# Optimization experiments

Hardware: AMD Instinct MI355X
Metric: run time of the kernel (lower is better)

The kernel has to match this reference:

```python
import jax, jax.numpy as jnp
import numpy as np

B, T, D = 2, 4096, 512
H = 8  # heads; head_dim = D // H = 64


def setup_inputs() -> dict:
    key = jax.random.key(0)
    ks = jax.random.split(key, 8)
    s = 0.02
    return {
        "queries": jax.random.normal(ks[0], (B, T, D), jnp.float32),
        "keys": jax.random.normal(ks[1], (B, T, D), jnp.float32),
        "values": jax.random.normal(ks[2], (B, T, D), jnp.float32),
        "Wq": jax.random.normal(ks[3], (D, D), jnp.float32) * s,
        "Wk": jax.random.normal(ks[4], (D, D), jnp.float32) * s,
        "Wv": jax.random.normal(ks[5], (D, D), jnp.float32) * s,
        "Wo": jax.random.normal(ks[6], (D, D), jnp.float32) * s,
        "bo": jnp.zeros((D,), jnp.float32),
    }


def reference(queries, keys, values, Wq, Wk, Wv, Wo, bo):
    # pad_dim = 0 for in_dim=512, n_heads=8, so no padding needed.
    Bq, Tq, _ = queries.shape
    Ts = keys.shape[1]
    hd = D // H
    # torch Linear: x @ W.T
    q = (queries @ Wq.T).reshape(Bq, Tq, H, hd).transpose(0, 2, 1, 3)  # [B,H,T,hd]
    k = (keys @ Wk.T).reshape(Bq, Ts, H, hd).transpose(0, 2, 1, 3)
    v = (values @ Wv.T).reshape(Bq, Ts, H, hd).transpose(0, 2, 1, 3)
    attn = jnp.einsum("bhtd,bhsd->bhts", q, k) / np.sqrt(hd).astype(np.float32)
    attn = jax.nn.softmax(attn, axis=-1)  # [B,H,T,Ts]
    z = jnp.einsum("bhts,bhsd->bhtd", attn, v)
    z = z.transpose(0, 2, 1, 3).reshape(Bq, Tq, D)
    out = z @ Wo.T + bo
    return (out, attn)
```

## Files before the change

### kernel.cpp

```cpp
#include <hip/hip_runtime.h>

typedef __attribute__((ext_vector_type(8))) short bf16x8;
typedef __attribute__((ext_vector_type(8))) unsigned short u16x8;
typedef __attribute__((ext_vector_type(4))) float f32x4;
typedef __attribute__((ext_vector_type(2))) unsigned uint2v;
typedef __attribute__((ext_vector_type(4))) unsigned uint4v;

#define DEVINL __device__ __forceinline__

constexpr int TB = 2;
constexpr int TT = 4096;
constexpr int TD = 512;
constexpr int TH = 8;
constexpr int THD = 64;
constexpr int TM = TB * TT;

DEVINL unsigned short f2b(float f) {
  unsigned u = __builtin_bit_cast(unsigned, f);
  u += 0x7FFFu + ((u >> 16) & 1u);
  return (unsigned short)(u >> 16);
}

DEVINL unsigned cvtpk(float lo, float hi) {
  unsigned r;
  asm("v_cvt_pk_bf16_f32 %0, %1, %2" : "=v"(r) : "v"(lo), "v"(hi));
  return r;
}

DEVINL void lgkm_barrier() {
  asm volatile("s_waitcnt lgkmcnt(0)" ::: "memory");
  __builtin_amdgcn_s_barrier();
  __builtin_amdgcn_sched_barrier(0);
}

template<int MODE>
__global__ __launch_bounds__(256, 2)
void gemm_xwt(const float* __restrict__ X, const float* __restrict__ W,
              unsigned short* __restrict__ Yb, float* __restrict__ Yf,
              const float* __restrict__ bias)
{
  constexpr int K = TD, N = TD;
  __shared__ unsigned short As[128][72];
  __shared__ unsigned short Bs[128][72];

  const int t    = threadIdx.x;
  const int lane = t & 63, w = t >> 6;
  const int fr = lane & 15, fq = lane >> 4;
  const int wr = (w >> 1) * 64, wc = (w & 1) * 64;
  const int bm = blockIdx.x * 128, bn = blockIdx.y * 128;
  const int srow = t >> 1;
  const int skh  = (t & 1) * 32;

  f32x4 acc[4][4];
  #pragma unroll
  for (int i = 0; i < 4; ++i)
    #pragma unroll
    for (int j = 0; j < 4; ++j)
      acc[i][j] = f32x4{0.f, 0.f, 0.f, 0.f};

  for (int k0 = 0; k0 < K; k0 += 64) {
    const float* srcA = X + (size_t)(bm + srow) * K + k0 + skh;
    const float* srcB = W + (size_t)(bn + srow) * K + k0 + skh;
    #pragma unroll
    for (int i = 0; i < 4; ++i) {
      float4 a0 = ((const float4*)srcA)[2 * i];
      float4 a1 = ((const float4*)srcA)[2 * i + 1];
      u16x8 oa = {f2b(a0.x), f2b(a0.y), f2b(a0.z), f2b(a0.w),
                  f2b(a1.x), f2b(a1.y), f2b(a1.z), f2b(a1.w)};
      *(u16x8*)&As[srow][skh + i * 8] = oa;
      float4 b0 = ((const float4*)srcB)[2 * i];
      float4 b1 = ((const float4*)srcB)[2 * i + 1];
      u16x8 ob = {f2b(b0.x), f2b(b0.y), f2b(b0.z), f2b(b0.w),
                  f2b(b1.x), f2b(b1.y), f2b(b1.z), f2b(b1.w)};
      *(u16x8*)&Bs[srow][skh + i * 8] = ob;
    }
    __syncthreads();
    #pragma unroll
    for (int kk = 0; kk < 2; ++kk) {
      bf16x8 af[4], bfv[4];
      #pragma unroll
      for (int i = 0; i < 4; ++i)
        af[i] = *(const bf16x8*)&As[wr + i * 16 + fr][kk * 32 + fq * 8];
      #pragma unroll
      for (int j = 0; j < 4; ++j)
        bfv[j] = *(const bf16x8*)&Bs[wc + j * 16 + fr][kk * 32 + fq * 8];
      #pragma unroll
      for (int i = 0; i < 4; ++i)
        #pragma unroll
        for (int j = 0; j < 4; ++j) {
          if (MODE == 2)
            acc[i][j] = __builtin_amdgcn_mfma_f32_16x16x32_bf16(bfv[i], af[j], acc[i][j], 0, 0, 0);
          else
            acc[i][j] = __builtin_amdgcn_mfma_f32_16x16x32_bf16(af[i], bfv[j], acc[i][j], 0, 0, 0);
        }
    }
    __syncthreads();
  }

  #pragma unroll
  for (int i = 0; i < 4; ++i) {
    #pragma unroll
    for (int j = 0; j < 4; ++j) {
      #pragma unroll
      for (int ii = 0; ii < 4; ++ii) {
        float v = acc[i][j][ii];
        if (MODE == 2) {
          const int Nidx = bn + wc + i * 16 + fq * 4 + ii;
          const int Midx = bm + wr + j * 16 + fr;
          const int h = Nidx >> 6, d = Nidx & (THD - 1);
          const int b = Midx >> 12, tt = Midx & (TT - 1);
          Yb[((size_t)(b * TH + h) * THD + d) * TT + tt] = f2b(v);
        } else {
          const int gm = bm + wr + i * 16 + fq * 4 + ii;
          const int gn = bn + wc + j * 16 + fr;
          if (MODE == 1) Yf[(size_t)gm * N + gn] = v + bias[gn];
          else           Yb[(size_t)gm * N + gn] = f2b(v);
        }
      }
    }
  }
}

__global__ __launch_bounds__(256, 2)
void attn_fused(const unsigned short* __restrict__ Qb,
                const unsigned short* __restrict__ Kb,
                const unsigned short* __restrict__ VTg,
                float* __restrict__ attnO, float* __restrict__ Z)
{
  __shared__ __align__(16) char smem_[55552];
  auto Ks   = (unsigned short (*)[64][72])smem_;
  auto VTs  = (unsigned short (*)[64][72])(smem_ + 18432);
  float* Lred = (float*)(smem_ + 55296);
  auto Zs   = (float (*)[68])smem_;

  const int t    = threadIdx.x;
  const int lane = t & 63, w = t >> 6;
  const int fr = lane & 15, fq = lane >> 4;
  const int bh = blockIdx.y;
  const int b  = bh >> 3, h = bh & 7;
  const int q0 = blockIdx.x * 64;

  const size_t rowKV  = ((size_t)(b * TT)) * TD + h * THD;
  const size_t vtBase = (size_t)bh * THD * TT;

  const int tr = t >> 2;
  const int tc = (t & 3) * 16;

  auto loadK = [&](int kvt, u16x8& r0, u16x8& r1) {
    const unsigned short* src = Kb + rowKV + (size_t)(kvt * 64 + tr) * TD + tc;
    r0 = *(const u16x8*)src;
    r1 = *(const u16x8*)(src + 8);
  };
  auto loadVT = [&](int kvt, u16x8& r0, u16x8& r1) {
    const unsigned short* src = VTg + vtBase + (size_t)tr * TT + kvt * 64 + tc;
    r0 = *(const u16x8*)src;
    r1 = *(const u16x8*)(src + 8);
  };
  auto writeK = [&](int buf, const u16x8& r0, const u16x8& r1) {
    *(u16x8*)&Ks[buf][tr][tc]     = r0;
    *(u16x8*)&Ks[buf][tr][tc + 8] = r1;
  };
  auto writeVT = [&](int buf, const u16x8& r0, const u16x8& r1) {
    *(u16x8*)&VTs[buf][tr][tc]     = r0;
    *(u16x8*)&VTs[buf][tr][tc + 8] = r1;
  };

  bf16x8 aq[4][2];
  #pragma unroll
  for (int qf = 0; qf < 4; ++qf) {
    const unsigned short* qsrc =
        Qb + ((size_t)(b * TT + q0 + qf * 16 + fr)) * TD + h * THD;
    aq[qf][0] = *(const bf16x8*)(qsrc + fq * 8);
    aq[qf][1] = *(const bf16x8*)(qsrc + 32 + fq * 8);
  }

  constexpr int NT = TT / 64;
  constexpr float K2 = 0.18033688011112042f;

  u16x8 kr0, kr1, vr0, vr1;
  loadK(0, kr0, kr1);
  writeK(0, kr0, kr1);
  lgkm_barrier();

  float lsum[4] = {0.f, 0.f, 0.f, 0.f};
  for (int j = 0; j < NT; ++j) {
    const int cur = j & 1;
    if (j + 1 < NT) loadK(j + 1, kr0, kr1);
    bf16x8 ak0 = *(const bf16x8*)&Ks[cur][w * 16 + fr][fq * 8];
    bf16x8 ak1 = *(const bf16x8*)&Ks[cur][w * 16 + fr][32 + fq * 8];
    __builtin_amdgcn_s_setprio(1);
    #pragma unroll
    for (int qf = 0; qf < 4; ++qf) {
      f32x4 s = f32x4{0.f, 0.f, 0.f, 0.f};
      s = __builtin_amdgcn_mfma_f32_16x16x32_bf16(ak0, aq[qf][0], s, 0, 0, 0);
      s = __builtin_amdgcn_mfma_f32_16x16x32_bf16(ak1, aq[qf][1], s, 0, 0, 0);
      #pragma unroll
      for (int i = 0; i < 4; ++i)
        lsum[qf] += __builtin_amdgcn_exp2f(s[i] * K2);
    }
    __builtin_amdgcn_s_setprio(0);
    if (j + 1 < NT) writeK(cur ^ 1, kr0, kr1);
    lgkm_barrier();
  }
  #pragma unroll
  for (int qf = 0; qf < 4; ++qf) {
    lsum[qf] += __shfl_xor(lsum[qf], 16, 64);
    lsum[qf] += __shfl_xor(lsum[qf], 32, 64);
  }
  if (fq == 0) {
    #pragma unroll
    for (int qf = 0; qf < 4; ++qf)
      Lred[(w * 4 + qf) * 16 + fr] = lsum[qf];
  }
  __syncthreads();
  float l2i[4];
  #pragma unroll
  for (int qf = 0; qf < 4; ++qf) {
    float s = Lred[(0 * 4 + qf) * 16 + fr] + Lred[(1 * 4 + qf) * 16 + fr] +
              Lred[(2 * 4 + qf) * 16 + fr] + Lred[(3 * 4 + qf) * 16 + fr];
    l2i[qf] = -__log2f(s);
  }

  loadK(0, kr0, kr1);
  loadVT(0, vr0, vr1);
  writeK(0, kr0, kr1);
  writeVT(0, vr0, vr1);
  lgkm_barrier();

  f32x4 accz[4][4];
  #pragma unroll
  for (int i = 0; i < 4; ++i)
    #pragma unroll
    for (int j = 0; j < 4; ++j)
      accz[i][j] = f32x4{0.f, 0.f, 0.f, 0.f};

  unsigned pa[4][4];

#define QK_TILE(J, HALF)                                                       \
  {                                                                            \
    if ((J) + 1 < NT) { loadK((J) + 1, kr0, kr1); loadVT((J) + 1, vr0, vr1); } \
    bf16x8 ak0 = *(const bf16x8*)&Ks[(J) & 1][w * 16 + fr][fq * 8];            \
    bf16x8 ak1 = *(const bf16x8*)&Ks[(J) & 1][w * 16 + fr][32 + fq * 8];       \
    __builtin_amdgcn_s_setprio(1);                                             \
    _Pragma("unroll")                                                          \
    for (int qf = 0; qf < 4; ++qf) {                                           \
      f32x4 s = f32x4{0.f, 0.f, 0.f, 0.f};                                     \
      s = __builtin_amdgcn_mfma_f32_16x16x32_bf16(ak0, aq[qf][0], s, 0, 0, 0); \
      s = __builtin_amdgcn_mfma_f32_16x16x32_bf16(ak1, aq[qf][1], s, 0, 0, 0); \
      float p0 = __builtin_amdgcn_exp2f(fmaf(s[0], K2, l2i[qf]));              \
      float p1 = __builtin_amdgcn_exp2f(fmaf(s[1], K2, l2i[qf]));              \
      float p2 = __builtin_amdgcn_exp2f(fmaf(s[2], K2, l2i[qf]));              \
      float p3 = __builtin_amdgcn_exp2f(fmaf(s[3], K2, l2i[qf]));              \
      f32x4 pv4 = {p0, p1, p2, p3};                                            \
      __builtin_nontemporal_store(pv4,                                         \
        (f32x4*)(attnO + ((size_t)bh * TT + q0 + qf * 16 + fr) * TT            \
                 + (J) * 64 + w * 16 + fq * 4));                               \
      pa[qf][(HALF) * 2 + 0] = cvtpk(p0, p1);                                  \
      pa[qf][(HALF) * 2 + 1] = cvtpk(p2, p3);                                  \
    }                                                                          \
    __builtin_amdgcn_s_setprio(0);                                             \
  }
#define STAGE_TAIL(J)                                                          \
  {                                                                            \
    if ((J) + 1 < NT) {                                                        \
      writeK(((J) + 1) & 1, kr0, kr1);                                         \
      writeVT(((J) + 1) & 3, vr0, vr1);                                        \
    }                                                                          \
    lgkm_barrier();                                                            \
  }

  for (int jp = 0; jp < NT / 2; ++jp) {
    const int j0 = jp * 2;
    const int vb = (jp & 1) * 2;
    QK_TILE(j0, 0)
    STAGE_TAIL(j0)
    QK_TILE(j0 + 1, 1)
    __builtin_amdgcn_s_setprio(1);
    #pragma unroll
    for (int df = 0; df < 4; ++df) {
      uint2v lo = *(const uint2v*)&VTs[vb][df * 16 + fr][w * 16 + fq * 4];
      uint2v hi = *(const uint2v*)&VTs[vb + 1][df * 16 + fr][w * 16 + fq * 4];
      uint4v bvv = {lo[0], lo[1], hi[0], hi[1]};
      bf16x8 bv = __builtin_bit_cast(bf16x8, bvv);
      #pragma unroll
      for (int qf = 0; qf < 4; ++qf) {
        uint4v pav = {pa[qf][0], pa[qf][1], pa[qf][2], pa[qf][3]};
        accz[qf][df] = __builtin_amdgcn_mfma_f32_16x16x32_bf16(
            __builtin_bit_cast(bf16x8, pav), bv, accz[qf][df], 0, 0, 0);
      }
    }
    __builtin_amdgcn_s_setprio(0);
    STAGE_TAIL(j0 + 1)
  }
#undef QK_TILE
#undef STAGE_TAIL

  for (int ww = 0; ww < 4; ++ww) {
    if (w == ww) {
      #pragma unroll
      for (int qf = 0; qf < 4; ++qf)
        #pragma unroll
        for (int df = 0; df < 4; ++df)
          #pragma unroll
          for (int i = 0; i < 4; ++i) {
            float* zp = &Zs[qf * 16 + fq * 4 + i][df * 16 + fr];
            float v = accz[qf][df][i];
            if (ww != 0) v += *zp;
            *zp = v;
          }
    }
    __syncthreads();
  }
  {
    const int r = t >> 2, c4 = (t & 3) * 16;
    float* zdst = Z + (size_t)(b * TT + q0 + r) * TD + h * THD + c4;
    #pragma unroll
    for (int i = 0; i < 4; ++i)
      *(f32x4*)(zdst + i * 4) = *(const f32x4*)&Zs[r][c4 + i * 4];
  }
}

extern "C" void kernel_launch(void* const* d_in, const int* in_sizes, int n_in,
                              void* d_out, int out_size, void* d_ws, size_t ws_size,
                              hipStream_t stream) {
  const float* queries = (const float*)d_in[0];
  const float* keys    = (const float*)d_in[1];
  const float* values  = (const float*)d_in[2];
  const float* Wq = (const float*)d_in[3];
  const float* Wk = (const float*)d_in[4];
  const float* Wv = (const float*)d_in[5];
  const float* Wo = (const float*)d_in[6];
  const float* bo = (const float*)d_in[7];

  float* out  = (float*)d_out;
  float* attn = out + (size_t)TM * TD;

  unsigned short* qb = (unsigned short*)d_ws;
  unsigned short* kb = qb + (size_t)TM * TD;
  unsigned short* vt = kb + (size_t)TM * TD;
  float*          zf = (float*)(vt + (size_t)TM * TD);

  dim3 gg(TM / 128, TD / 128), bb(256);
  gemm_xwt<0><<<gg, bb, 0, stream>>>(queries, Wq, qb, nullptr, nullptr);
  gemm_xwt<0><<<gg, bb, 0, stream>>>(keys,    Wk, kb, nullptr, nullptr);
  gemm_xwt<2><<<gg, bb, 0, stream>>>(values,  Wv, vt, nullptr, nullptr);

  attn_fused<<<dim3(TT / 64, TB * TH), bb, 0, stream>>>(qb, kb, vt, attn, zf);

  gemm_xwt<1><<<gg, bb, 0, stream>>>(zf, Wo, nullptr, out, bo);
}
```

Measured before the change: 542.9 us.

## Split KV range across waves and load K/V directly from global memory

```diff
diff --git a/kernel.cpp b/kernel.cpp
--- a/kernel.cpp
+++ b/kernel.cpp
@@ -25,12 +25,6 @@
   unsigned r;
   asm("v_cvt_pk_bf16_f32 %0, %1, %2" : "=v"(r) : "v"(lo), "v"(hi));
   return r;
-}
-
-DEVINL void lgkm_barrier() {
-  asm volatile("s_waitcnt lgkmcnt(0)" ::: "memory");
-  __builtin_amdgcn_s_barrier();
-  __builtin_amdgcn_sched_barrier(0);
 }
 
 template<int MODE>
@@ -127,11 +121,8 @@
                 const unsigned short* __restrict__ VTg,
                 float* __restrict__ attnO, float* __restrict__ Z)
 {
-  __shared__ __align__(16) char smem_[55552];
-  auto Ks   = (unsigned short (*)[64][72])smem_;
-  auto VTs  = (unsigned short (*)[64][72])(smem_ + 18432);
-  float* Lred = (float*)(smem_ + 55296);
-  auto Zs   = (float (*)[68])smem_;
+  __shared__ float Lred[4][4][16];
+  __shared__ float Zs[64][68];
 
   const int t    = threadIdx.x;
   const int lane = t & 63, w = t >> 6;
@@ -143,28 +134,6 @@
   const size_t rowKV  = ((size_t)(b * TT)) * TD + h * THD;
   const size_t vtBase = (size_t)bh * THD * TT;
 
-  const int tr = t >> 2;
-  const int tc = (t & 3) * 16;
-
-  auto loadK = [&](int kvt, u16x8& r0, u16x8& r1) {
-    const unsigned short* src = Kb + rowKV + (size_t)(kvt * 64 + tr) * TD + tc;
-    r0 = *(const u16x8*)src;
-    r1 = *(const u16x8*)(src + 8);
-  };
-  auto loadVT = [&](int kvt, u16x8& r0, u16x8& r1) {
-    const unsigned short* src = VTg + vtBase + (size_t)tr * TT + kvt * 64 + tc;
-    r0 = *(const u16x8*)src;
-    r1 = *(const u16x8*)(src + 8);
-  };
-  auto writeK = [&](int buf, const u16x8& r0, const u16x8& r1) {
-    *(u16x8*)&Ks[buf][tr][tc]     = r0;
-    *(u16x8*)&Ks[buf][tr][tc + 8] = r1;
-  };
-  auto writeVT = [&](int buf, const u16x8& r0, const u16x8& r1) {
-    *(u16x8*)&VTs[buf][tr][tc]     = r0;
-    *(u16x8*)&VTs[buf][tr][tc + 8] = r1;
-  };
-
   bf16x8 aq[4][2];
   #pragma unroll
   for (int qf = 0; qf < 4; ++qf) {
@@ -174,33 +143,36 @@
     aq[qf][1] = *(const bf16x8*)(qsrc + 32 + fq * 8);
   }
 
-  constexpr int NT = TT / 64;
   constexpr float K2 = 0.18033688011112042f;
 
-  u16x8 kr0, kr1, vr0, vr1;
-  loadK(0, kr0, kr1);
-  writeK(0, kr0, kr1);
-  lgkm_barrier();
+  const unsigned short* kbase = Kb + rowKV + (size_t)fr * TD + fq * 8;
+  const int kvw = w * 1024;
+  constexpr size_t CSTR = (size_t)16 * TD;
 
   float lsum[4] = {0.f, 0.f, 0.f, 0.f};
-  for (int j = 0; j < NT; ++j) {
-    const int cur = j & 1;
-    if (j + 1 < NT) loadK(j + 1, kr0, kr1);
-    bf16x8 ak0 = *(const bf16x8*)&Ks[cur][w * 16 + fr][fq * 8];
-    bf16x8 ak1 = *(const bf16x8*)&Ks[cur][w * 16 + fr][32 + fq * 8];
-    __builtin_amdgcn_s_setprio(1);
-    #pragma unroll
-    for (int qf = 0; qf < 4; ++qf) {
-      f32x4 s = f32x4{0.f, 0.f, 0.f, 0.f};
-      s = __builtin_amdgcn_mfma_f32_16x16x32_bf16(ak0, aq[qf][0], s, 0, 0, 0);
-      s = __builtin_amdgcn_mfma_f32_16x16x32_bf16(ak1, aq[qf][1], s, 0, 0, 0);
-      #pragma unroll
-      for (int i = 0; i < 4; ++i)
-        lsum[qf] += __builtin_amdgcn_exp2f(s[i] * K2);
-    }
-    __builtin_amdgcn_s_setprio(0);
-    if (j + 1 < NT) writeK(cur ^ 1, kr0, kr1);
-    lgkm_barrier();
+  {
+    const unsigned short* kp = kbase + (size_t)kvw * TD;
+    u16x8 kn0 = *(const u16x8*)kp;
+    u16x8 kn1 = *(const u16x8*)(kp + 32);
+    for (int c = 0; c < 64; ++c) {
+      bf16x8 ak0 = __builtin_bit_cast(bf16x8, kn0);
+      bf16x8 ak1 = __builtin_bit_cast(bf16x8, kn1);
+      if (c + 1 < 64) {
+        const unsigned short* np = kp + (size_t)(c + 1) * CSTR;
+        kn0 = *(const u16x8*)np;
+        kn1 = *(const u16x8*)(np + 32);
+      }
+      #pragma unroll
+      for (int qf = 0; qf < 4; ++qf) {
+        f32x4 s = f32x4{0.f, 0.f, 0.f, 0.f};
+        s = __builtin_amdgcn_mfma_f32_16x16x32_bf16(ak0, aq[qf][0], s, 0, 0, 0);
+        s = __builtin_amdgcn_mfma_f32_16x16x32_bf16(ak1, aq[qf][1], s, 0, 0, 0);
+        lsum[qf] += __builtin_amdgcn_exp2f(s[0] * K2) +
+                    __builtin_amdgcn_exp2f(s[1] * K2) +
+                    __builtin_amdgcn_exp2f(s[2] * K2) +
+                    __builtin_amdgcn_exp2f(s[3] * K2);
+      }
+    }
   }
   #pragma unroll
   for (int qf = 0; qf < 4; ++qf) {
@@ -209,23 +181,16 @@
   }
   if (fq == 0) {
     #pragma unroll
-    for (int qf = 0; qf < 4; ++qf)
-      Lred[(w * 4 + qf) * 16 + fr] = lsum[qf];
+    for (int qf = 0; qf < 4; ++qf) Lred[w][qf][fr] = lsum[qf];
   }
   __syncthreads();
   float l2i[4];
   #pragma unroll
   for (int qf = 0; qf < 4; ++qf) {
-    float s = Lred[(0 * 4 + qf) * 16 + fr] + Lred[(1 * 4 + qf) * 16 + fr] +
-              Lred[(2 * 4 + qf) * 16 + fr] + Lred[(3 * 4 + qf) * 16 + fr];
+    float s = Lred[0][qf][fr] + Lred[1][qf][fr] +
+              Lred[2][qf][fr] + Lred[3][qf][fr];
     l2i[qf] = -__log2f(s);
   }
-
-  loadK(0, kr0, kr1);
-  loadVT(0, vr0, vr1);
-  writeK(0, kr0, kr1);
-  writeVT(0, vr0, vr1);
-  lgkm_barrier();
 
   f32x4 accz[4][4];
   #pragma unroll
@@ -234,53 +199,57 @@
     for (int j = 0; j < 4; ++j)
       accz[i][j] = f32x4{0.f, 0.f, 0.f, 0.f};
 
-  unsigned pa[4][4];
-
-#define QK_TILE(J, HALF)                                                       \
-  {                                                                            \
-    if ((J) + 1 < NT) { loadK((J) + 1, kr0, kr1); loadVT((J) + 1, vr0, vr1); } \
-    bf16x8 ak0 = *(const bf16x8*)&Ks[(J) & 1][w * 16 + fr][fq * 8];            \
-    bf16x8 ak1 = *(const bf16x8*)&Ks[(J) & 1][w * 16 + fr][32 + fq * 8];       \
-    __builtin_amdgcn_s_setprio(1);                                             \
-    _Pragma("unroll")                                                          \
-    for (int qf = 0; qf < 4; ++qf) {                                           \
-      f32x4 s = f32x4{0.f, 0.f, 0.f, 0.f};                                     \
-      s = __builtin_amdgcn_mfma_f32_16x16x32_bf16(ak0, aq[qf][0], s, 0, 0, 0); \
-      s = __builtin_amdgcn_mfma_f32_16x16x32_bf16(ak1, aq[qf][1], s, 0, 0, 0); \
-      float p0 = __builtin_amdgcn_exp2f(fmaf(s[0], K2, l2i[qf]));              \
-      float p1 = __builtin_amdgcn_exp2f(fmaf(s[1], K2, l2i[qf]));              \
-      float p2 = __builtin_amdgcn_exp2f(fmaf(s[2], K2, l2i[qf]));              \
-      float p3 = __builtin_amdgcn_exp2f(fmaf(s[3], K2, l2i[qf]));              \
-      f32x4 pv4 = {p0, p1, p2, p3};                                            \
-      __builtin_nontemporal_store(pv4,                                         \
-        (f32x4*)(attnO + ((size_t)bh * TT + q0 + qf * 16 + fr) * TT            \
-                 + (J) * 64 + w * 16 + fq * 4));                               \
-      pa[qf][(HALF) * 2 + 0] = cvtpk(p0, p1);                                  \
-      pa[qf][(HALF) * 2 + 1] = cvtpk(p2, p3);                                  \
-    }                                                                          \
-    __builtin_amdgcn_s_setprio(0);                                             \
-  }
-#define STAGE_TAIL(J)                                                          \
-  {                                                                            \
-    if ((J) + 1 < NT) {                                                        \
-      writeK(((J) + 1) & 1, kr0, kr1);                                         \
-      writeVT(((J) + 1) & 3, vr0, vr1);                                        \
-    }                                                                          \
-    lgkm_barrier();                                                            \
-  }
-
-  for (int jp = 0; jp < NT / 2; ++jp) {
-    const int j0 = jp * 2;
-    const int vb = (jp & 1) * 2;
-    QK_TILE(j0, 0)
-    STAGE_TAIL(j0)
-    QK_TILE(j0 + 1, 1)
-    __builtin_amdgcn_s_setprio(1);
+  float* abase = attnO + ((size_t)bh * TT + q0 + fr) * TT + fq * 4;
+  const unsigned short* vbase = VTg + vtBase + (size_t)fr * TT + fq * 4;
+
+  for (int pr = 0; pr < 32; ++pr) {
+    const int kvb0 = kvw + pr * 32;
+    const unsigned short* kp0 = kbase + (size_t)kvb0 * TD;
+    const unsigned short* kp1 = kp0 + CSTR;
+    u16x8 a00 = *(const u16x8*)kp0;
+    u16x8 a01 = *(const u16x8*)(kp0 + 32);
+    u16x8 a10 = *(const u16x8*)kp1;
+    u16x8 a11 = *(const u16x8*)(kp1 + 32);
+    uint2v vlo[4], vhi[4];
     #pragma unroll
     for (int df = 0; df < 4; ++df) {
-      uint2v lo = *(const uint2v*)&VTs[vb][df * 16 + fr][w * 16 + fq * 4];
-      uint2v hi = *(const uint2v*)&VTs[vb + 1][df * 16 + fr][w * 16 + fq * 4];
-      uint4v bvv = {lo[0], lo[1], hi[0], hi[1]};
+      const unsigned short* vp = vbase + (size_t)df * 16 * TT + kvb0;
+      vlo[df] = *(const uint2v*)vp;
+      vhi[df] = *(const uint2v*)(vp + 16);
+    }
+
+    unsigned pa[4][4];
+    #pragma unroll
+    for (int qf = 0; qf < 4; ++qf) {
+      f32x4 s = f32x4{0.f, 0.f, 0.f, 0.f};
+      s = __builtin_amdgcn_mfma_f32_16x16x32_bf16(__builtin_bit_cast(bf16x8, a00), aq[qf][0], s, 0, 0, 0);
+      s = __builtin_amdgcn_mfma_f32_16x16x32_bf16(__builtin_bit_cast(bf16x8, a01), aq[qf][1], s, 0, 0, 0);
+      float p0 = __builtin_amdgcn_exp2f(fmaf(s[0], K2, l2i[qf]));
+      float p1 = __builtin_amdgcn_exp2f(fmaf(s[1], K2, l2i[qf]));
+      float p2 = __builtin_amdgcn_exp2f(fmaf(s[2], K2, l2i[qf]));
+      float p3 = __builtin_amdgcn_exp2f(fmaf(s[3], K2, l2i[qf]));
+      f32x4 pv4 = {p0, p1, p2, p3};
+      __builtin_nontemporal_store(pv4, (f32x4*)(abase + (size_t)qf * 16 * TT + kvb0));
+      pa[qf][0] = cvtpk(p0, p1);
+      pa[qf][1] = cvtpk(p2, p3);
+    }
+    #pragma unroll
+    for (int qf = 0; qf < 4; ++qf) {
+      f32x4 s = f32x4{0.f, 0.f, 0.f, 0.f};
+      s = __builtin_amdgcn_mfma_f32_16x16x32_bf16(__builtin_bit_cast(bf16x8, a10), aq[qf][0], s, 0, 0, 0);
+      s = __builtin_amdgcn_mfma_f32_16x16x32_bf16(__builtin_bit_cast(bf16x8, a11), aq[qf][1], s, 0, 0, 0);
+      float p0 = __builtin_amdgcn_exp2f(fmaf(s[0], K2, l2i[qf]));
+      float p1 = __builtin_amdgcn_exp2f(fmaf(s[1], K2, l2i[qf]));
+      float p2 = __builtin_amdgcn_exp2f(fmaf(s[2], K2, l2i[qf]));
+      float p3 = __builtin_amdgcn_exp2f(fmaf(s[3], K2, l2i[qf]));
+      f32x4 pv4 = {p0, p1, p2, p3};
+      __builtin_nontemporal_store(pv4, (f32x4*)(abase + (size_t)qf * 16 * TT + kvb0 + 16));
+      pa[qf][2] = cvtpk(p0, p1);
+      pa[qf][3] = cvtpk(p2, p3);
+    }
+    #pragma unroll
+    for (int df = 0; df < 4; ++df) {
+      uint4v bvv = {vlo[df][0], vlo[df][1], vhi[df][0], vhi[df][1]};
       bf16x8 bv = __builtin_bit_cast(bf16x8, bvv);
       #pragma unroll
       for (int qf = 0; qf < 4; ++qf) {
@@ -289,11 +258,7 @@
             __builtin_bit_cast(bf16x8, pav), bv, accz[qf][df], 0, 0, 0);
       }
     }
-    __builtin_amdgcn_s_setprio(0);
-    STAGE_TAIL(j0 + 1)
-  }
-#undef QK_TILE
-#undef STAGE_TAIL
+  }
 
   for (int ww = 0; ww < 4; ++ww) {
     if (w == ww) {
```

After: 612.6 us. +12.8%, slower.
